# Optimization experiments

Hardware: AMD Instinct MI355X
Metric: run time of the kernel (lower is better)

The kernel has to match this reference:

```python
import jax, jax.numpy as jnp
import numpy as np

ALPHA = 0.2  # LeakyReLU negative slope (pyGAT default)
NEG_INF = -9e15


def setup_inputs() -> dict:
    key = jax.random.key(0)
    ks = jax.random.split(key, 8)
    N, IN, OUT, H, C = 4096, 512, 64, 8, 10
    x = jax.random.normal(ks[0], (N, IN), dtype=jnp.float32)
    adj = jax.random.randint(ks[1], (N, N), 0, 2, dtype=jnp.int32)
    W = jax.random.normal(ks[2], (H, IN, OUT), dtype=jnp.float32) * 0.05
    a1 = jax.random.normal(ks[3], (H, OUT), dtype=jnp.float32) * 0.05
    a2 = jax.random.normal(ks[4], (H, OUT), dtype=jnp.float32) * 0.05
    Wo = jax.random.normal(ks[5], (H * OUT, C), dtype=jnp.float32) * 0.05
    ao1 = jax.random.normal(ks[6], (C,), dtype=jnp.float32) * 0.05
    ao2 = jax.random.normal(ks[7], (C,), dtype=jnp.float32) * 0.05
    return {"x": x, "adj": adj, "W": W, "a1": a1, "a2": a2,
            "Wo": Wo, "ao1": ao1, "ao2": ao2}


def _multi_head_gat(h, mask, W, a1, a2):
    # h: [N, F_in], W: [H, F_in, F_out], a1/a2: [H, F_out], mask: [N, N] bool
    Wh = jnp.einsum('ni,hio->hno', h, W)            # [H, N, F_out]
    f1 = jnp.einsum('hno,ho->hn', Wh, a1)           # [H, N]
    f2 = jnp.einsum('hno,ho->hn', Wh, a2)           # [H, N]
    e = f1[:, :, None] + f2[:, None, :]             # [H, N, N]
    e = jnp.where(e > 0, e, ALPHA * e)              # LeakyReLU(0.2)
    e = jnp.where(mask[None, :, :], e, NEG_INF)     # adjacency mask
    attn = jax.nn.softmax(e, axis=-1)               # [H, N, N]
    return jnp.einsum('hnm,hmo->hno', attn, Wh)     # [H, N, F_out]


def reference(x, adj, W, a1, a2, Wo, ao1, ao2):
    mask = adj > 0
    # hidden heads (concat=True -> ELU on concatenated output)
    heads = _multi_head_gat(x, mask, W, a1, a2)          # [H, N, O]
    H, N, O = heads.shape
    hcat = jnp.transpose(heads, (1, 0, 2)).reshape(N, H * O)
    hcat = jax.nn.elu(hcat)
    # output layer (concat=False -> no ELU)
    out = _multi_head_gat(hcat, mask, Wo[None], ao1[None], ao2[None])[0]  # [N, C]
    return jax.nn.log_softmax(out, axis=-1)
```

## Files before the change

### kernel.cpp

```cpp
#include <hip/hip_runtime.h>
#include <hip/hip_bf16.h>

typedef __bf16 bf16x8 __attribute__((ext_vector_type(8)));
typedef short short8 __attribute__((ext_vector_type(8)));
typedef float f32x4 __attribute__((ext_vector_type(4)));

union BF8 { short8 s; bf16x8 b; };

#define N_NODES 4096
#define F_IN 512
#define F_OUT 64
#define NHEAD 8
#define HID 512
#define NCLS 10
#define GAT_ALPHA 0.2f
#define MSPLIT 4
#define WST 4096
#define NWORD (N_NODES / 64)
#define RB 32
#define CB 64
#define NIT ((N_NODES / MSPLIT) / CB)
#define RB2 16
#define MS2 8
#define MT2 (N_NODES / MS2 / 64)

__device__ inline unsigned short f2bf(float f) {
  unsigned u = __builtin_bit_cast(unsigned, f);
  unsigned r = (u + 0x7FFFu + ((u >> 16) & 1u)) >> 16;
  return (unsigned short)r;
}
__device__ inline float bf2f(unsigned short h) {
  unsigned u = ((unsigned)h) << 16;
  return __builtin_bit_cast(float, u);
}

__global__ __launch_bounds__(256) void pack_adj_kernel(
    const int* __restrict__ adj, unsigned long long* __restrict__ bits) {
  int wid = blockIdx.x * 4 + (threadIdx.x >> 6);
  int l = threadIdx.x & 63;
  unsigned long long m = __ballot(adj[(size_t)wid * 64 + l] != 0);
  if (l == 0) bits[wid] = m;
}

__global__ __launch_bounds__(256) void gemm1_kernel(
    const float* __restrict__ x, const float* __restrict__ W,
    const float* __restrict__ a1, const float* __restrict__ a2,
    unsigned short* __restrict__ WhbT, float* __restrict__ rho1,
    float* __restrict__ E2, float* __restrict__ E2s) {
  __shared__ short As[64 * 40];
  __shared__ short Bs[64 * 40];
  const int bx = blockIdx.x;
  const int h  = blockIdx.y;
  const int t  = threadIdx.x;
  const int w  = t >> 6, l = t & 63;
  const int lr = l & 15, ls = l >> 4;
  f32x4 acc[4] = {};
  for (int k0 = 0; k0 < F_IN; k0 += 32) {
    {
      int r = t >> 2, c0 = (t & 3) * 8;
      const float* src = x + (bx * 64 + r) * F_IN + k0 + c0;
      float4 v0 = *(const float4*)src;
      float4 v1 = *(const float4*)(src + 4);
      short8 sv;
      sv[0]=f2bf(v0.x); sv[1]=f2bf(v0.y); sv[2]=f2bf(v0.z); sv[3]=f2bf(v0.w);
      sv[4]=f2bf(v1.x); sv[5]=f2bf(v1.y); sv[6]=f2bf(v1.z); sv[7]=f2bf(v1.w);
      *(short8*)&As[r * 40 + c0] = sv;
    }
    {
      int kk = t >> 3, o0 = (t & 7) * 8;
      const float* src = W + ((h * F_IN) + k0 + kk) * F_OUT + o0;
      float4 v0 = *(const float4*)src;
      float4 v1 = *(const float4*)(src + 4);
      float vv[8] = {v0.x, v0.y, v0.z, v0.w, v1.x, v1.y, v1.z, v1.w};
      #pragma unroll
      for (int i = 0; i < 8; ++i) Bs[(o0 + i) * 40 + kk] = f2bf(vv[i]);
    }
    __syncthreads();
    BF8 a; a.s = *(short8*)&As[(w * 16 + lr) * 40 + ls * 8];
    #pragma unroll
    for (int fc = 0; fc < 4; ++fc) {
      BF8 b; b.s = *(short8*)&Bs[(fc * 16 + lr) * 40 + ls * 8];
      acc[fc] = __builtin_amdgcn_mfma_f32_16x16x32_bf16(a.b, b.b, acc[fc], 0, 0, 0);
    }
    __syncthreads();
  }
  #pragma unroll
  for (int fc = 0; fc < 4; ++fc)
    #pragma unroll
    for (int j = 0; j < 4; ++j) {
      int row = bx * 64 + w * 16 + ls * 4 + j;
      int col = fc * 16 + lr;
      WhbT[(size_t)(h * F_OUT + col) * WST + row] = f2bf(acc[fc][j]);
    }
  float a1c[4], a2c[4];
  #pragma unroll
  for (int fc = 0; fc < 4; ++fc) {
    a1c[fc] = a1[h * F_OUT + fc * 16 + lr];
    a2c[fc] = a2[h * F_OUT + fc * 16 + lr];
  }
  #pragma unroll
  for (int j = 0; j < 4; ++j) {
    float s1 = 0.f, s2 = 0.f;
    #pragma unroll
    for (int fc = 0; fc < 4; ++fc) { s1 += acc[fc][j] * a1c[fc]; s2 += acc[fc][j] * a2c[fc]; }
    #pragma unroll
    for (int off = 1; off <= 8; off <<= 1) {
      s1 += __shfl_xor(s1, off, 64);
      s2 += __shfl_xor(s2, off, 64);
    }
    if (lr == 0) {
      int row = bx * 64 + w * 16 + ls * 4 + j;
      int idx = h * N_NODES + row;
      rho1[idx] = __expf((GAT_ALPHA - 1.f) * s1);
      E2[idx]   = __expf(s2);
      E2s[idx]  = __expf(GAT_ALPHA * s2);
    }
  }
}

__global__ __launch_bounds__(512, 4) void att1_kernel(
    const unsigned long long* __restrict__ adjbits,
    const float* __restrict__ rho1,
    const float* __restrict__ E2, const float* __restrict__ E2s,
    const unsigned short* __restrict__ WhbT,
    float* __restrict__ accP, float* __restrict__ SP) {
  __shared__ __align__(16) short Bt[NHEAD][64 * CB];
  const int nb = blockIdx.x * RB;
  const int q  = blockIdx.y;
  const int t  = threadIdx.x;
  const int h  = t >> 6;
  const int l  = t & 63;
  const int r  = l & 15, s = l >> 4;

  const float rho0  = rho1[h * N_NODES + nb + r];
  const float rho1v = rho1[h * N_NODES + nb + 16 + r];
  const float* __restrict__ E2h  = E2  + h * N_NODES;
  const float* __restrict__ E2sh = E2s + h * N_NODES;
  const unsigned long long* __restrict__ ab0 = adjbits + (size_t)(nb + r) * NWORD;
  const unsigned long long* __restrict__ ab1 = adjbits + (size_t)(nb + 16 + r) * NWORD;

  const unsigned short* gsrc0 =
      WhbT + (size_t)(h * F_OUT + (l >> 3)) * WST + (((l & 7) ^ (l >> 3)) * 8);

  const int tb0 = q * (N_NODES / MSPLIT);

  #pragma unroll
  for (int i = 0; i < 8; ++i)
    __builtin_amdgcn_global_load_lds(
        (const __attribute__((address_space(1))) void*)(gsrc0 + tb0 + (size_t)(i * 8) * WST),
        (__attribute__((address_space(3))) void*)&Bt[h][i * 512], 16, 0, 0);

  float S0 = 0.f, S1 = 0.f;
  f32x4 acc[2][4] = {};
  for (int it = 0; it < NIT; ++it) {
    const int tb = tb0 + it * CB;
    const unsigned long long mk0 = ab0[tb >> 6];
    const unsigned long long mk1 = ab1[tb >> 6];
    BF8 a0[2], a1f[2];
    #pragma unroll
    for (int kf = 0; kf < 2; ++kf) {
      const int cb = tb + kf * 32 + s * 8;
      float4 ea = *(const float4*)(E2h + cb);
      float4 eb = *(const float4*)(E2h + cb + 4);
      float4 sa = *(const float4*)(E2sh + cb);
      float4 sb = *(const float4*)(E2sh + cb + 4);
      float ev[8] = {ea.x, ea.y, ea.z, ea.w, eb.x, eb.y, eb.z, eb.w};
      float sv[8] = {sa.x, sa.y, sa.z, sa.w, sb.x, sb.y, sb.z, sb.w};
      const unsigned b0m = (unsigned)(mk0 >> (kf * 32 + s * 8)) & 0xffu;
      const unsigned b1m = (unsigned)(mk1 >> (kf * 32 + s * 8)) & 0xffu;
      #pragma unroll
      for (int j = 0; j < 8; ++j) {
        float q0 = fmaxf(ev[j], rho0 * sv[j]);
        q0 = ((b0m >> j) & 1u) ? q0 : 0.f;
        S0 += q0; a0[kf].b[j] = (__bf16)q0;
        float q1 = fmaxf(ev[j], rho1v * sv[j]);
        q1 = ((b1m >> j) & 1u) ? q1 : 0.f;
        S1 += q1; a1f[kf].b[j] = (__bf16)q1;
      }
    }
    asm volatile("s_waitcnt vmcnt(0)" ::: "memory");
    BF8 b[2][4];
    #pragma unroll
    for (int kf = 0; kf < 2; ++kf)
      #pragma unroll
      for (int fc = 0; fc < 4; ++fc)
        b[kf][fc].s = *(short8*)&Bt[h][(fc * 16 + r) * CB + ((kf * 32 + s * 8) ^ ((r & 7) * 8))];
    asm volatile("s_waitcnt lgkmcnt(0)" ::: "memory");
    __builtin_amdgcn_sched_barrier(0);
    if (it + 1 < NIT) {
      #pragma unroll
      for (int i = 0; i < 8; ++i)
        __builtin_amdgcn_global_load_lds(
            (const __attribute__((address_space(1))) void*)(gsrc0 + tb + CB + (size_t)(i * 8) * WST),
            (__attribute__((address_space(3))) void*)&Bt[h][i * 512], 16, 0, 0);
    }
    __builtin_amdgcn_sched_barrier(0);
    #pragma unroll
    for (int kf = 0; kf < 2; ++kf)
      #pragma unroll
      for (int fc = 0; fc < 4; ++fc) {
        acc[0][fc] = __builtin_amdgcn_mfma_f32_16x16x32_bf16(a0[kf].b,  b[kf][fc].b, acc[0][fc], 0, 0, 0);
        acc[1][fc] = __builtin_amdgcn_mfma_f32_16x16x32_bf16(a1f[kf].b, b[kf][fc].b, acc[1][fc], 0, 0, 0);
      }
  }

  S0 += __shfl_xor(S0, 16, 64); S0 += __shfl_xor(S0, 32, 64);
  S1 += __shfl_xor(S1, 16, 64); S1 += __shfl_xor(S1, 32, 64);
  if (s == 0) {
    SP[((size_t)q * NHEAD + h) * N_NODES + nb + r]      = S0;
    SP[((size_t)q * NHEAD + h) * N_NODES + nb + 16 + r] = S1;
  }
  #pragma unroll
  for (int rg = 0; rg < 2; ++rg)
    #pragma unroll
    for (int fc = 0; fc < 4; ++fc)
      #pragma unroll
      for (int j = 0; j < 4; ++j) {
        int n = nb + rg * 16 + s * 4 + j;
        int col = h * F_OUT + fc * 16 + r;
        accP[((size_t)q * N_NODES + n) * HID + col] = acc[rg][fc][j];
      }
}

__global__ __launch_bounds__(256) void gemm2_kernel(
    const float* __restrict__ accP, const float* __restrict__ SP,
    const float* __restrict__ Wo,
    const float* __restrict__ ao1, const float* __restrict__ ao2,
    unsigned short* __restrict__ Wh2T, float* __restrict__ rho_o,
    float* __restrict__ Eg2, float* __restrict__ Eg2s) {
  int n = blockIdx.x * 4 + (threadIdx.x >> 6);
  int l = threadIdx.x & 63;
  const int h = l >> 3;
  float Ssum = 0.f;
  #pragma unroll
  for (int q = 0; q < MSPLIT; ++q) Ssum += SP[((size_t)q * NHEAD + h) * N_NODES + n];
  float v[8] = {};
  #pragma unroll
  for (int q = 0; q < MSPLIT; ++q) {
    const float* row = accP + ((size_t)q * N_NODES + n) * HID + l * 8;
    float4 va = *(const float4*)row;
    float4 vb = *(const float4*)(row + 4);
    v[0] += va.x; v[1] += va.y; v[2] += va.z; v[3] += va.w;
    v[4] += vb.x; v[5] += vb.y; v[6] += vb.z; v[7] += vb.w;
  }
  float rs = 1.0f / Ssum;
  float acc[NCLS] = {};
  #pragma unroll
  for (int j = 0; j < 8; ++j) {
    float e = v[j] * rs;
    e = e > 0.f ? e : (__expf(e) - 1.0f);
    float hv = bf2f(f2bf(e));
    const float* wrow = Wo + (l * 8 + j) * NCLS;
    #pragma unroll
    for (int c = 0; c < NCLS; ++c) acc[c] += hv * wrow[c];
  }
  #pragma unroll
  for (int c = 0; c < NCLS; ++c)
    #pragma unroll
    for (int off = 32; off > 0; off >>= 1) acc[c] += __shfl_xor(acc[c], off, 64);
  if (l == 0) {
    float s1 = 0.f, s2 = 0.f;
    #pragma unroll
    for (int c = 0; c < NCLS; ++c) {
      s1 += acc[c] * ao1[c];
      s2 += acc[c] * ao2[c];
    }
    #pragma unroll
    for (int c = 0; c < 16; ++c)
      Wh2T[(size_t)c * N_NODES + n] = (c < NCLS) ? f2bf(acc[c]) : (unsigned short)0;
    rho_o[n] = __expf((GAT_ALPHA - 1.f) * s1);
    Eg2[n]   = __expf(s2);
    Eg2s[n]  = __expf(GAT_ALPHA * s2);
  }
}

__global__ __launch_bounds__(512) void att2_kernel(
    const unsigned long long* __restrict__ adjbits,
    const float* __restrict__ rho_o,
    const float* __restrict__ Eg2, const float* __restrict__ Eg2s,
    const unsigned short* __restrict__ Wh2T, float* __restrict__ out) {
  __shared__ float Lacc[MS2][RB2][16];
  __shared__ float LS[MS2][RB2];
  const int nb = blockIdx.x * RB2;
  const int t  = threadIdx.x;
  const int w  = t >> 6;
  const int l  = t & 63;
  const int r  = l & 15, s = l >> 4;
  const int row = nb + r;
  const float ro = rho_o[row];
  const unsigned long long* __restrict__ ab = adjbits + (size_t)row * NWORD;
  const int tb0 = w * (N_NODES / MS2);

  float S = 0.f;
  f32x4 acc = {};
  for (int it = 0; it < MT2; ++it) {
    const int tb = tb0 + it * 64;
    const unsigned long long mk = ab[tb >> 6];
    BF8 a0[2], b0[2];
    #pragma unroll
    for (int kf = 0; kf < 2; ++kf) {
      const int cb = tb + kf * 32 + s * 8;
      b0[kf].s = *(const short8*)(Wh2T + (size_t)r * N_NODES + cb);
      float4 ea = *(const float4*)(Eg2 + cb);
      float4 eb = *(const float4*)(Eg2 + cb + 4);
      float4 sa = *(const float4*)(Eg2s + cb);
      float4 sb = *(const float4*)(Eg2s + cb + 4);
      float ev[8] = {ea.x, ea.y, ea.z, ea.w, eb.x, eb.y, eb.z, eb.w};
      float sv[8] = {sa.x, sa.y, sa.z, sa.w, sb.x, sb.y, sb.z, sb.w};
      const unsigned bm = (unsigned)(mk >> (kf * 32 + s * 8)) & 0xffu;
      #pragma unroll
      for (int j = 0; j < 8; ++j) {
        float qv = fmaxf(ev[j], ro * sv[j]);
        qv = ((bm >> j) & 1u) ? qv : 0.f;
        S += qv;
        a0[kf].b[j] = (__bf16)qv;
      }
    }
    #pragma unroll
    for (int kf = 0; kf < 2; ++kf)
      acc = __builtin_amdgcn_mfma_f32_16x16x32_bf16(a0[kf].b, b0[kf].b, acc, 0, 0, 0);
  }
  S += __shfl_xor(S, 16, 64);
  S += __shfl_xor(S, 32, 64);
  if (s == 0) LS[w][r] = S;
  #pragma unroll
  for (int j = 0; j < 4; ++j) Lacc[w][s * 4 + j][r] = acc[j];
  __syncthreads();
  if (t < 256) {
    const int rr = t >> 4, cc = t & 15;
    float Ssum = 0.f, vsum = 0.f;
    #pragma unroll
    for (int q = 0; q < MS2; ++q) { Ssum += LS[q][rr]; vsum += Lacc[q][rr][cc]; }
    float lo = vsum / Ssum;
    float lom = (cc < NCLS) ? lo : -1e30f;
    float mx = lom;
    #pragma unroll
    for (int off = 1; off <= 8; off <<= 1) mx = fmaxf(mx, __shfl_xor(mx, off, 64));
    float ex = (cc < NCLS) ? __expf(lo - mx) : 0.f;
    float se = ex;
    #pragma unroll
    for (int off = 1; off <= 8; off <<= 1) se += __shfl_xor(se, off, 64);
    float lse = mx + __logf(se);
    if (cc < NCLS) out[(size_t)(nb + rr) * NCLS + cc] = lo - lse;
  }
}

extern "C" void kernel_launch(void* const* d_in, const int* in_sizes, int n_in,
                              void* d_out, int out_size, void* d_ws, size_t ws_size,
                              hipStream_t stream) {
  (void)in_sizes; (void)n_in; (void)out_size; (void)ws_size;
  const float* x   = (const float*)d_in[0];
  const int*   adj = (const int*)d_in[1];
  const float* W   = (const float*)d_in[2];
  const float* a1  = (const float*)d_in[3];
  const float* a2  = (const float*)d_in[4];
  const float* Wo  = (const float*)d_in[5];
  const float* ao1 = (const float*)d_in[6];
  const float* ao2 = (const float*)d_in[7];
  float* out = (float*)d_out;

  char* ws = (char*)d_ws;
  unsigned long long* adjbits = (unsigned long long*)ws; ws += (size_t)N_NODES * NWORD * 8;
  unsigned short* WhbT= (unsigned short*)ws; ws += (size_t)HID * WST * 2;
  float* accP         = (float*)ws;          ws += (size_t)MSPLIT * N_NODES * HID * 4;
  float* SP           = (float*)ws;          ws += (size_t)MSPLIT * NHEAD * N_NODES * 4;
  float* rho1         = (float*)ws;          ws += (size_t)NHEAD * N_NODES * 4;
  float* E2           = (float*)ws;          ws += (size_t)NHEAD * N_NODES * 4;
  float* E2s          = (float*)ws;          ws += (size_t)NHEAD * N_NODES * 4;
  unsigned short* Wh2T= (unsigned short*)ws; ws += (size_t)16 * N_NODES * 2;
  float* rho_o        = (float*)ws;          ws += (size_t)N_NODES * 4;
  float* Eg2          = (float*)ws;          ws += (size_t)N_NODES * 4;
  float* Eg2s         = (float*)ws;          ws += (size_t)N_NODES * 4;

  pack_adj_kernel<<<N_NODES * NWORD / 4, 256, 0, stream>>>(adj, adjbits);
  gemm1_kernel<<<dim3(64, 8), 256, 0, stream>>>(x, W, a1, a2, WhbT, rho1, E2, E2s);
  att1_kernel<<<dim3(N_NODES / RB, MSPLIT), 512, 0, stream>>>(adjbits, rho1, E2, E2s, WhbT, accP, SP);
  gemm2_kernel<<<N_NODES / 4, 256, 0, stream>>>(accP, SP, Wo, ao1, ao2, Wh2T, rho_o, Eg2, Eg2s);
  att2_kernel<<<N_NODES / RB2, 512, 0, stream>>>(adjbits, rho_o, Eg2, Eg2s, Wh2T, out);
}
```

Before: 128.3 us.

## Switch layer-1 attention to packed fp16 math and fp16 MFMA

The exponent tables E2/E2s are now stored as fp16, halving their load traffic in att1. The attention weights are computed with packed half2 multiply/max, masked bitwise, and summed with fdot2, which cuts VALU work per element. Wh is stored as fp16 so the MFMAs become f16, and gemm1 writes the transposed Wh through an LDS tile as vectorised row stores instead of scattered 2-byte stores. The risk is fp16 overflow or underflow in the exp values, which have a much narrower range than the bf16/fp32 used before.

```diff
diff --git a/kernel.cpp b/kernel.cpp
--- a/kernel.cpp
+++ b/kernel.cpp
@@ -1,11 +1,16 @@
 #include <hip/hip_runtime.h>
 #include <hip/hip_bf16.h>
+#include <hip/hip_fp16.h>
 
 typedef __bf16 bf16x8 __attribute__((ext_vector_type(8)));
+typedef _Float16 h8_t __attribute__((ext_vector_type(8)));
+typedef _Float16 v2h __attribute__((ext_vector_type(2)));
 typedef short short8 __attribute__((ext_vector_type(8)));
 typedef float f32x4 __attribute__((ext_vector_type(4)));
 
 union BF8 { short8 s; bf16x8 b; };
+union H8  { short8 s; h8_t h; unsigned w[4]; };
+union HU  { _Float16 f; unsigned short u; };
 
 #define N_NODES 4096
 #define F_IN 512
@@ -24,6 +29,15 @@
 #define MS2 8
 #define MT2 (N_NODES / MS2 / 64)
 
+#if defined(__has_builtin)
+#if __has_builtin(__builtin_amdgcn_fdot2)
+#define FDOT2(a, b, c) __builtin_amdgcn_fdot2((a), (b), (c), false)
+#endif
+#endif
+#ifndef FDOT2
+#define FDOT2(a, b, c) ((c) + (float)(a)[0] * (float)(b)[0] + (float)(a)[1] * (float)(b)[1])
+#endif
+
 __device__ inline unsigned short f2bf(float f) {
   unsigned u = __builtin_bit_cast(unsigned, f);
   unsigned r = (u + 0x7FFFu + ((u >> 16) & 1u)) >> 16;
@@ -46,9 +60,10 @@
     const float* __restrict__ x, const float* __restrict__ W,
     const float* __restrict__ a1, const float* __restrict__ a2,
     unsigned short* __restrict__ WhbT, float* __restrict__ rho1,
-    float* __restrict__ E2, float* __restrict__ E2s) {
+    unsigned short* __restrict__ E2f16, unsigned short* __restrict__ E2sf16) {
   __shared__ short As[64 * 40];
   __shared__ short Bs[64 * 40];
+  __shared__ short Ts[64 * 72];
   const int bx = blockIdx.x;
   const int h  = blockIdx.y;
   const int t  = threadIdx.x;
@@ -88,10 +103,18 @@
   for (int fc = 0; fc < 4; ++fc)
     #pragma unroll
     for (int j = 0; j < 4; ++j) {
-      int row = bx * 64 + w * 16 + ls * 4 + j;
-      int col = fc * 16 + lr;
-      WhbT[(size_t)(h * F_OUT + col) * WST + row] = f2bf(acc[fc][j]);
-    }
+      HU hu; hu.f = (_Float16)acc[fc][j];
+      Ts[(fc * 16 + lr) * 72 + (w * 16 + ls * 4 + j)] = (short)hu.u;
+    }
+  __syncthreads();
+  {
+    int col = t >> 2, seg = t & 3;
+    short8 o0 = *(short8*)&Ts[col * 72 + seg * 16];
+    short8 o1 = *(short8*)&Ts[col * 72 + seg * 16 + 8];
+    unsigned short* dst = WhbT + (size_t)(h * F_OUT + col) * WST + bx * 64 + seg * 16;
+    *(short8*)dst = o0;
+    *(short8*)(dst + 8) = o1;
+  }
   float a1c[4], a2c[4];
   #pragma unroll
   for (int fc = 0; fc < 4; ++fc) {
@@ -112,8 +135,10 @@
       int row = bx * 64 + w * 16 + ls * 4 + j;
       int idx = h * N_NODES + row;
       rho1[idx] = __expf((GAT_ALPHA - 1.f) * s1);
-      E2[idx]   = __expf(s2);
-      E2s[idx]  = __expf(GAT_ALPHA * s2);
+      HU u1; u1.f = (_Float16)__expf(s2);
+      HU u2; u2.f = (_Float16)__expf(GAT_ALPHA * s2);
+      E2f16[idx]  = u1.u;
+      E2sf16[idx] = u2.u;
     }
   }
 }
@@ -121,7 +146,7 @@
 __global__ __launch_bounds__(512, 4) void att1_kernel(
     const unsigned long long* __restrict__ adjbits,
     const float* __restrict__ rho1,
-    const float* __restrict__ E2, const float* __restrict__ E2s,
+    const unsigned short* __restrict__ E2f16, const unsigned short* __restrict__ E2sf16,
     const unsigned short* __restrict__ WhbT,
     float* __restrict__ accP, float* __restrict__ SP) {
   __shared__ __align__(16) short Bt[NHEAD][64 * CB];
@@ -134,8 +159,11 @@
 
   const float rho0  = rho1[h * N_NODES + nb + r];
   const float rho1v = rho1[h * N_NODES + nb + 16 + r];
-  const float* __restrict__ E2h  = E2  + h * N_NODES;
-  const float* __restrict__ E2sh = E2s + h * N_NODES;
+  const v2h rh0 = {(_Float16)rho0, (_Float16)rho0};
+  const v2h rh1 = {(_Float16)rho1v, (_Float16)rho1v};
+  const v2h ones = {(_Float16)1.0f, (_Float16)1.0f};
+  const unsigned short* __restrict__ E2h  = E2f16  + h * N_NODES;
+  const unsigned short* __restrict__ E2sh = E2sf16 + h * N_NODES;
   const unsigned long long* __restrict__ ab0 = adjbits + (size_t)(nb + r) * NWORD;
   const unsigned long long* __restrict__ ab1 = adjbits + (size_t)(nb + 16 + r) * NWORD;
 
@@ -156,30 +184,34 @@
     const int tb = tb0 + it * CB;
     const unsigned long long mk0 = ab0[tb >> 6];
     const unsigned long long mk1 = ab1[tb >> 6];
-    BF8 a0[2], a1f[2];
+    H8 a0[2], a1f[2];
     #pragma unroll
     for (int kf = 0; kf < 2; ++kf) {
       const int cb = tb + kf * 32 + s * 8;
-      float4 ea = *(const float4*)(E2h + cb);
-      float4 eb = *(const float4*)(E2h + cb + 4);
-      float4 sa = *(const float4*)(E2sh + cb);
-      float4 sb = *(const float4*)(E2sh + cb + 4);
-      float ev[8] = {ea.x, ea.y, ea.z, ea.w, eb.x, eb.y, eb.z, eb.w};
-      float sv[8] = {sa.x, sa.y, sa.z, sa.w, sb.x, sb.y, sb.z, sb.w};
-      const unsigned b0m = (unsigned)(mk0 >> (kf * 32 + s * 8)) & 0xffu;
-      const unsigned b1m = (unsigned)(mk1 >> (kf * 32 + s * 8)) & 0xffu;
-      #pragma unroll
-      for (int j = 0; j < 8; ++j) {
-        float q0 = fmaxf(ev[j], rho0 * sv[j]);
-        q0 = ((b0m >> j) & 1u) ? q0 : 0.f;
-        S0 += q0; a0[kf].b[j] = (__bf16)q0;
-        float q1 = fmaxf(ev[j], rho1v * sv[j]);
-        q1 = ((b1m >> j) & 1u) ? q1 : 0.f;
-        S1 += q1; a1f[kf].b[j] = (__bf16)q1;
+      uint4 ew = *(const uint4*)(E2h + cb);
+      uint4 sw = *(const uint4*)(E2sh + cb);
+      const unsigned ewa[4] = {ew.x, ew.y, ew.z, ew.w};
+      const unsigned swa[4] = {sw.x, sw.y, sw.z, sw.w};
+      const unsigned bm0 = (unsigned)(mk0 >> (kf * 32 + s * 8)) & 0xffu;
+      const unsigned bm1 = (unsigned)(mk1 >> (kf * 32 + s * 8)) & 0xffu;
+      #pragma unroll
+      for (int p = 0; p < 4; ++p) {
+        const v2h e2 = __builtin_bit_cast(v2h, ewa[p]);
+        const v2h es = __builtin_bit_cast(v2h, swa[p]);
+        const unsigned lo0 = ((bm0 >> (2 * p)) & 1u) ? 0x0000FFFFu : 0u;
+        const unsigned hi0 = ((bm0 >> (2 * p + 1)) & 1u) ? 0xFFFF0000u : 0u;
+        unsigned q0w = __builtin_bit_cast(unsigned, __builtin_elementwise_max(e2, (v2h)(rh0 * es))) & (lo0 | hi0);
+        S0 = FDOT2(__builtin_bit_cast(v2h, q0w), ones, S0);
+        a0[kf].w[p] = q0w;
+        const unsigned lo1 = ((bm1 >> (2 * p)) & 1u) ? 0x0000FFFFu : 0u;
+        const unsigned hi1 = ((bm1 >> (2 * p + 1)) & 1u) ? 0xFFFF0000u : 0u;
+        unsigned q1w = __builtin_bit_cast(unsigned, __builtin_elementwise_max(e2, (v2h)(rh1 * es))) & (lo1 | hi1);
+        S1 = FDOT2(__builtin_bit_cast(v2h, q1w), ones, S1);
+        a1f[kf].w[p] = q1w;
       }
     }
     asm volatile("s_waitcnt vmcnt(0)" ::: "memory");
-    BF8 b[2][4];
+    H8 b[2][4];
     #pragma unroll
     for (int kf = 0; kf < 2; ++kf)
       #pragma unroll
@@ -199,8 +231,8 @@
     for (int kf = 0; kf < 2; ++kf)
       #pragma unroll
       for (int fc = 0; fc < 4; ++fc) {
-        acc[0][fc] = __builtin_amdgcn_mfma_f32_16x16x32_bf16(a0[kf].b,  b[kf][fc].b, acc[0][fc], 0, 0, 0);
-        acc[1][fc] = __builtin_amdgcn_mfma_f32_16x16x32_bf16(a1f[kf].b, b[kf][fc].b, acc[1][fc], 0, 0, 0);
+        acc[0][fc] = __builtin_amdgcn_mfma_f32_16x16x32_f16(a0[kf].h,  b[kf][fc].h, acc[0][fc], 0, 0, 0);
+        acc[1][fc] = __builtin_amdgcn_mfma_f32_16x16x32_f16(a1f[kf].h, b[kf][fc].h, acc[1][fc], 0, 0, 0);
       }
   }
 
@@ -365,16 +397,16 @@
   float* accP         = (float*)ws;          ws += (size_t)MSPLIT * N_NODES * HID * 4;
   float* SP           = (float*)ws;          ws += (size_t)MSPLIT * NHEAD * N_NODES * 4;
   float* rho1         = (float*)ws;          ws += (size_t)NHEAD * N_NODES * 4;
-  float* E2           = (float*)ws;          ws += (size_t)NHEAD * N_NODES * 4;
-  float* E2s          = (float*)ws;          ws += (size_t)NHEAD * N_NODES * 4;
+  unsigned short* E2f16  = (unsigned short*)ws; ws += (size_t)NHEAD * N_NODES * 2;
+  unsigned short* E2sf16 = (unsigned short*)ws; ws += (size_t)NHEAD * N_NODES * 2;
   unsigned short* Wh2T= (unsigned short*)ws; ws += (size_t)16 * N_NODES * 2;
   float* rho_o        = (float*)ws;          ws += (size_t)N_NODES * 4;
   float* Eg2          = (float*)ws;          ws += (size_t)N_NODES * 4;
   float* Eg2s         = (float*)ws;          ws += (size_t)N_NODES * 4;
 
   pack_adj_kernel<<<N_NODES * NWORD / 4, 256, 0, stream>>>(adj, adjbits);
-  gemm1_kernel<<<dim3(64, 8), 256, 0, stream>>>(x, W, a1, a2, WhbT, rho1, E2, E2s);
-  att1_kernel<<<dim3(N_NODES / RB, MSPLIT), 512, 0, stream>>>(adjbits, rho1, E2, E2s, WhbT, accP, SP);
+  gemm1_kernel<<<dim3(64, 8), 256, 0, stream>>>(x, W, a1, a2, WhbT, rho1, E2f16, E2sf16);
+  att1_kernel<<<dim3(N_NODES / RB, MSPLIT), 512, 0, stream>>>(adjbits, rho1, E2f16, E2sf16, WhbT, accP, SP);
   gemm2_kernel<<<N_NODES / 4, 256, 0, stream>>>(accP, SP, Wo, ao1, ao2, Wh2T, rho_o, Eg2, Eg2s);
   att2_kernel<<<N_NODES / RB2, 512, 0, stream>>>(adjbits, rho_o, Eg2, Eg2s, Wh2T, out);
 }
```

New measurement: 119.5 us. 1.07x faster.
